# Kernel tuning notes

Hardware: AMD Instinct MI355X
Metric: run time of the kernel (lower is better)

The kernel has to match this reference:

```python
import jax, jax.numpy as jnp
import numpy as np


def setup_inputs() -> dict:
    key = jax.random.key(0)
    k1, k2, k3 = jax.random.split(key, 3)
    B, Cin, H, W = 64, 16, 256, 256
    Cout, K = 64, 3
    x = jax.random.normal(k1, (B, Cin, H, W), dtype=jnp.float32)
    # PyTorch Conv2d init scale ~ 1/sqrt(fan_in)
    fan_in = Cin * K * K
    conv_weight = jax.random.normal(k2, (Cout, Cin, K, K), dtype=jnp.float32) / np.sqrt(fan_in)
    conv_bias = jax.random.normal(k3, (Cout,), dtype=jnp.float32) / np.sqrt(fan_in)
    return {"x": x, "conv_weight": conv_weight, "conv_bias": conv_bias}


def reference(x, conv_weight, conv_bias):
    # Conv2d: stride=1, padding=0 (VALID), dilation=1, groups=1
    y = jax.lax.conv_general_dilated(
        x, conv_weight,
        window_strides=(1, 1),
        padding="VALID",
        dimension_numbers=("NCHW", "OIHW", "NCHW"),
    ) + conv_bias[None, :, None, None]          # [B, Cout, 254, 254]
    m = jnp.min(y, axis=1, keepdims=True)        # [B, 1, 254, 254] min over channels
    return jnp.tanh(jnp.tanh(m))                 # double tanh
```

## Files before the change

### kernel.cpp

```cpp
#include <hip/hip_runtime.h>
#include <math.h>

#define CIN    16
#define COUT   64
#define H      256
#define W      256
#define OH     254
#define OW     254
#define NTAP   9
#define NSTRIP 8
#define RING   6

typedef _Float16 f16x8  __attribute__((ext_vector_type(8)));
typedef float    f32x16 __attribute__((ext_vector_type(16)));

#define XSLOT(w, g) ((((w) << 1) | (g)) ^ (((w) >> 2) & 7))

__global__ void wpack_kernel(const float* __restrict__ w, _Float16* __restrict__ wpk) {
    int idx = blockIdx.x * 256 + threadIdx.x;
    if (idx >= NTAP * 2 * 64 * 8) return;
    int e = idx & 7, l = (idx >> 3) & 63, m = (idx >> 9) & 1, t = idx >> 10;
    int co  = (l & 31) + 32 * m;
    int cin = 8 * (l >> 5) + e;
    wpk[idx] = (_Float16)w[((co * CIN + cin) * 3 + t / 3) * 3 + (t % 3)];
}

__device__ __forceinline__ float tanh_fast(float v) {
    float e = __expf(2.0f * v);
    return 1.0f - 2.0f * __builtin_amdgcn_rcpf(e + 1.0f);
}

__global__ __launch_bounds__(256, 2) void conv_mfma_kernel(
        const float* __restrict__ x, const f16x8* __restrict__ wpk,
        const float* __restrict__ bias, float* __restrict__ out) {
    __shared__ f16x8 xs[RING * 512];
    __shared__ f16x8 wv[NTAP * 2 * 64];

    const int tid = threadIdx.x;
    int bid = blockIdx.x;
    int nb  = (bid & 7) * 64 + (bid >> 3);
    int b   = nb >> 3;
    int s   = nb & 7;
    const int npairs = (s == NSTRIP - 1) ? 15 : 16;
    const int oh0 = s * 32;

    const float* xb = x + (size_t)b * CIN * H * W;

    for (int i = tid; i < NTAP * 2 * 64; i += 256) wv[i] = wpk[i];

    const int rsel = tid >> 7;
    const int w2   = (tid & 127) * 2;

    #pragma unroll
    for (int pass = 0; pass < 2; ++pass) {
        int row = oh0 + 2 * pass + rsel;
        const float* p = xb + (size_t)row * W + w2;
        float2 vv[16];
        #pragma unroll
        for (int c = 0; c < 16; ++c) vv[c] = *(const float2*)(p + (size_t)c * H * W);
        int ring = 2 * pass + rsel;
        #pragma unroll
        for (int g = 0; g < 2; ++g)
            #pragma unroll
            for (int o = 0; o < 2; ++o) {
                f16x8 q;
                #pragma unroll
                for (int e = 0; e < 8; ++e)
                    q[e] = (_Float16)(o == 0 ? vv[8 * g + e].x : vv[8 * g + e].y);
                xs[ring * 512 + XSLOT(w2 + o, g)] = q;
            }
    }
    __syncthreads();

    const int lane = tid & 63;
    const int wave = tid >> 6;
    const int ohl  = wave >> 1;
    const int ph   = (wave & 1) * 128;
    const int l31  = lane & 31;
    const int g2   = lane >> 5;

    int off[3][4];
    #pragma unroll
    for (int kw = 0; kw < 3; ++kw)
        #pragma unroll
        for (int n = 0; n < 4; ++n) {
            int w = ph + 32 * n + l31 + kw;
            if (w > 255) w = 255;
            off[kw][n] = XSLOT(w, g2);
        }

    float binit[2][16];
    #pragma unroll
    for (int m = 0; m < 2; ++m)
        #pragma unroll
        for (int r = 0; r < 16; ++r)
            binit[m][r] = bias[(r & 3) + 8 * (r >> 2) + 4 * g2 + 32 * m];

    f32x16 acc[2][4];
    #pragma unroll
    for (int m = 0; m < 2; ++m)
        #pragma unroll
        for (int n = 0; n < 4; ++n)
            #pragma unroll
            for (int r = 0; r < 16; ++r)
                acc[m][n][r] = binit[m][r];

    for (int p = 0; p < npairs; ++p) {
        float2 vv[16];
        const bool pf = (p + 1 < npairs);
        if (pf) {
            int row = oh0 + 2 * p + 4 + rsel;
            const float* pp = xb + (size_t)row * W + w2;
            #pragma unroll
            for (int c = 0; c < 16; ++c) vv[c] = *(const float2*)(pp + (size_t)c * H * W);
        }

        int hb = 2 * p + ohl;
        int r0 = hb % RING, r1 = (hb + 1) % RING, r2 = (hb + 2) % RING;
        const f16x8* xr0 = xs + r0 * 512;
        const f16x8* xr1 = xs + r1 * 512;
        const f16x8* xr2 = xs + r2 * 512;

        #pragma unroll
        for (int t = 0; t < NTAP; ++t) {
            const int kh = t / 3, kw = t % 3;
            f16x8 a0 = wv[(t * 2 + 0) * 64 + lane];
            f16x8 a1 = wv[(t * 2 + 1) * 64 + lane];
            const f16x8* xr = (kh == 0) ? xr0 : (kh == 1) ? xr1 : xr2;
            #pragma unroll
            for (int n = 0; n < 4; ++n) {
                f16x8 bf = xr[off[kw][n]];
                acc[0][n] = __builtin_amdgcn_mfma_f32_32x32x16_f16(a0, bf, acc[0][n], 0, 0, 0);
                acc[1][n] = __builtin_amdgcn_mfma_f32_32x32x16_f16(a1, bf, acc[1][n], 0, 0, 0);
            }
        }

        const int oh = oh0 + 2 * p + ohl;
        #pragma unroll
        for (int n = 0; n < 4; ++n) {
            float mn = fminf(acc[0][n][0], acc[1][n][0]);
            #pragma unroll
            for (int r = 1; r < 16; ++r)
                mn = fminf(mn, fminf(acc[0][n][r], acc[1][n][r]));
            mn = fminf(mn, __shfl_xor(mn, 32));
            float t2 = tanh_fast(tanh_fast(mn));
            int px = ph + 32 * n + l31;
            if (g2 == 0 && px < OW)
                out[((size_t)b * OH + oh) * OW + px] = t2;
            #pragma unroll
            for (int m = 0; m < 2; ++m)
                #pragma unroll
                for (int r = 0; r < 16; ++r)
                    acc[m][n][r] = binit[m][r];
        }

        if (pf) {
            int ring = (2 * p + 4 + rsel) % RING;
            #pragma unroll
            for (int g = 0; g < 2; ++g)
                #pragma unroll
                for (int o = 0; o < 2; ++o) {
                    f16x8 q;
                    #pragma unroll
                    for (int e = 0; e < 8; ++e)
                        q[e] = (_Float16)(o == 0 ? vv[8 * g + e].x : vv[8 * g + e].y);
                    xs[ring * 512 + XSLOT(w2 + o, g)] = q;
                }
        }
        __syncthreads();
    }
}

extern "C" void kernel_launch(void* const* d_in, const int* in_sizes, int n_in,
                              void* d_out, int out_size, void* d_ws, size_t ws_size,
                              hipStream_t stream) {
    const float* x    = (const float*)d_in[0];
    const float* w    = (const float*)d_in[1];
    const float* bias = (const float*)d_in[2];
    float* out = (float*)d_out;
    _Float16* wpk = (_Float16*)d_ws;

    wpack_kernel<<<36, 256, 0, stream>>>(w, wpk);
    conv_mfma_kernel<<<512, 256, 0, stream>>>(x, (const f16x8*)wpk, bias, out);
}
```

Measured before the change: 100.8 us.

## Restructure conv into 512-thread blocks with deeper LDS ring and fewer barriers

Blocks grow to 512 threads, and each block now covers 64 output rows of one image, giving 256 blocks instead of 512. The LDS ring grows from 6 to 10 rows, so the block-wide barrier runs only every other row-pair iteration, and staging is split by channel group across half-blocks. Weight fragments are held in registers instead of being re-read from LDS on every tap. Each wave now computes two 32-pixel column tiles instead of four, which frees accumulator registers but halves MFMA work per B-fragment read and leaves fewer blocks to balance across CUs.

```diff
diff --git a/kernel.cpp b/kernel.cpp
--- a/kernel.cpp
+++ b/kernel.cpp
@@ -8,8 +8,7 @@
 #define OH     254
 #define OW     254
 #define NTAP   9
-#define NSTRIP 8
-#define RING   6
+#define RING   10
 
 typedef _Float16 f16x8  __attribute__((ext_vector_type(8)));
 typedef float    f32x16 __attribute__((ext_vector_type(16)));
@@ -30,116 +29,116 @@
     return 1.0f - 2.0f * __builtin_amdgcn_rcpf(e + 1.0f);
 }
 
-__global__ __launch_bounds__(256, 2) void conv_mfma_kernel(
+__global__ __launch_bounds__(512, 2) void conv_mfma_kernel(
         const float* __restrict__ x, const f16x8* __restrict__ wpk,
         const float* __restrict__ bias, float* __restrict__ out) {
-    __shared__ f16x8 xs[RING * 512];
-    __shared__ f16x8 wv[NTAP * 2 * 64];
+    __shared__ f16x8 xs[RING * 512 + 64];
 
     const int tid = threadIdx.x;
-    int bid = blockIdx.x;
-    int nb  = (bid & 7) * 64 + (bid >> 3);
-    int b   = nb >> 3;
-    int s   = nb & 7;
-    const int npairs = (s == NSTRIP - 1) ? 15 : 16;
-    const int oh0 = s * 32;
+    const int b   = blockIdx.x >> 2;
+    const int s   = blockIdx.x & 3;
+    const int oh0 = s * 64;
+    const int npairs = (s == 3) ? 31 : 32;
 
     const float* xb = x + (size_t)b * CIN * H * W;
 
-    for (int i = tid; i < NTAP * 2 * 64; i += 256) wv[i] = wpk[i];
+    const int lane = tid & 63;
+    f16x8 wreg[NTAP][2];
+#pragma unroll
+    for (int t = 0; t < NTAP; ++t)
+#pragma unroll
+        for (int m = 0; m < 2; ++m)
+            wreg[t][m] = wpk[(t * 2 + m) * 64 + lane];
 
-    const int rsel = tid >> 7;
-    const int w2   = (tid & 127) * 2;
+    const int gld  = tid >> 8;
+    const int rld  = (tid >> 7) & 1;
+    const int pp   = tid & 127;
+    const int w2   = pp * 2;
 
-    #pragma unroll
-    for (int pass = 0; pass < 2; ++pass) {
-        int row = oh0 + 2 * pass + rsel;
-        const float* p = xb + (size_t)row * W + w2;
-        float2 vv[16];
-        #pragma unroll
-        for (int c = 0; c < 16; ++c) vv[c] = *(const float2*)(p + (size_t)c * H * W);
-        int ring = 2 * pass + rsel;
-        #pragma unroll
-        for (int g = 0; g < 2; ++g)
-            #pragma unroll
-            for (int o = 0; o < 2; ++o) {
-                f16x8 q;
-                #pragma unroll
-                for (int e = 0; e < 8; ++e)
-                    q[e] = (_Float16)(o == 0 ? vv[8 * g + e].x : vv[8 * g + e].y);
-                xs[ring * 512 + XSLOT(w2 + o, g)] = q;
-            }
+#define STAGE(rowAbs, slot)                                                     \
+    {                                                                           \
+        int row_ = (rowAbs) > 255 ? 255 : (rowAbs);                             \
+        const float* p_ = xb + (size_t)row_ * W + w2;                           \
+        float2 vv_[8];                                                          \
+        _Pragma("unroll")                                                       \
+        for (int c = 0; c < 8; ++c)                                             \
+            vv_[c] = *(const float2*)(p_ + (size_t)(8 * gld + c) * (H * W));    \
+        f16x8 q0, q1;                                                           \
+        _Pragma("unroll")                                                       \
+        for (int c = 0; c < 8; ++c) { q0[c] = (_Float16)vv_[c].x;               \
+                                      q1[c] = (_Float16)vv_[c].y; }             \
+        xs[(slot) * 512 + XSLOT(w2,     gld)] = q0;                             \
+        xs[(slot) * 512 + XSLOT(w2 + 1, gld)] = q1;                             \
     }
+
+#pragma unroll
+    for (int i = 0; i < 3; ++i)
+        STAGE(oh0 + 2 * i + rld, 2 * i + rld)
     __syncthreads();
 
-    const int lane = tid & 63;
     const int wave = tid >> 6;
-    const int ohl  = wave >> 1;
-    const int ph   = (wave & 1) * 128;
+    const int ohl  = wave >> 2;
+    const int ph   = (wave & 3) * 64;
     const int l31  = lane & 31;
     const int g2   = lane >> 5;
 
-    int off[3][4];
-    #pragma unroll
+    int off[3][2];
+#pragma unroll
     for (int kw = 0; kw < 3; ++kw)
-        #pragma unroll
-        for (int n = 0; n < 4; ++n) {
+#pragma unroll
+        for (int n = 0; n < 2; ++n) {
             int w = ph + 32 * n + l31 + kw;
             if (w > 255) w = 255;
             off[kw][n] = XSLOT(w, g2);
         }
 
     float binit[2][16];
-    #pragma unroll
+#pragma unroll
     for (int m = 0; m < 2; ++m)
-        #pragma unroll
+#pragma unroll
         for (int r = 0; r < 16; ++r)
             binit[m][r] = bias[(r & 3) + 8 * (r >> 2) + 4 * g2 + 32 * m];
 
-    f32x16 acc[2][4];
-    #pragma unroll
+    f32x16 acc[2][2];
+#pragma unroll
     for (int m = 0; m < 2; ++m)
-        #pragma unroll
-        for (int n = 0; n < 4; ++n)
-            #pragma unroll
+#pragma unroll
+        for (int n = 0; n < 2; ++n)
+#pragma unroll
             for (int r = 0; r < 16; ++r)
                 acc[m][n][r] = binit[m][r];
 
     for (int p = 0; p < npairs; ++p) {
-        float2 vv[16];
-        const bool pf = (p + 1 < npairs);
-        if (pf) {
-            int row = oh0 + 2 * p + 4 + rsel;
-            const float* pp = xb + (size_t)row * W + w2;
-            #pragma unroll
-            for (int c = 0; c < 16; ++c) vv[c] = *(const float2*)(pp + (size_t)c * H * W);
-        }
+        int ldrow = oh0 + 2 * p + 6 + rld;
+        if (ldrow > 255) ldrow = 255;
+        const float* lp = xb + (size_t)ldrow * W + w2;
+        float2 vv[8];
+#pragma unroll
+        for (int c = 0; c < 8; ++c)
+            vv[c] = *(const float2*)(lp + (size_t)(8 * gld + c) * (H * W));
 
-        int hb = 2 * p + ohl;
-        int r0 = hb % RING, r1 = (hb + 1) % RING, r2 = (hb + 2) % RING;
-        const f16x8* xr0 = xs + r0 * 512;
-        const f16x8* xr1 = xs + r1 * 512;
-        const f16x8* xr2 = xs + r2 * 512;
+        const int hb = 2 * p + ohl;
+        const f16x8* xr0 = xs + (hb % RING) * 512;
+        const f16x8* xr1 = xs + ((hb + 1) % RING) * 512;
+        const f16x8* xr2 = xs + ((hb + 2) % RING) * 512;
 
-        #pragma unroll
+#pragma unroll
         for (int t = 0; t < NTAP; ++t) {
             const int kh = t / 3, kw = t % 3;
-            f16x8 a0 = wv[(t * 2 + 0) * 64 + lane];
-            f16x8 a1 = wv[(t * 2 + 1) * 64 + lane];
             const f16x8* xr = (kh == 0) ? xr0 : (kh == 1) ? xr1 : xr2;
-            #pragma unroll
-            for (int n = 0; n < 4; ++n) {
+#pragma unroll
+            for (int n = 0; n < 2; ++n) {
                 f16x8 bf = xr[off[kw][n]];
-                acc[0][n] = __builtin_amdgcn_mfma_f32_32x32x16_f16(a0, bf, acc[0][n], 0, 0, 0);
-                acc[1][n] = __builtin_amdgcn_mfma_f32_32x32x16_f16(a1, bf, acc[1][n], 0, 0, 0);
+                acc[0][n] = __builtin_amdgcn_mfma_f32_32x32x16_f16(wreg[t][0], bf, acc[0][n], 0, 0, 0);
+                acc[1][n] = __builtin_amdgcn_mfma_f32_32x32x16_f16(wreg[t][1], bf, acc[1][n], 0, 0, 0);
             }
         }
 
         const int oh = oh0 + 2 * p + ohl;
-        #pragma unroll
-        for (int n = 0; n < 4; ++n) {
+#pragma unroll
+        for (int n = 0; n < 2; ++n) {
             float mn = fminf(acc[0][n][0], acc[1][n][0]);
-            #pragma unroll
+#pragma unroll
             for (int r = 1; r < 16; ++r)
                 mn = fminf(mn, fminf(acc[0][n][r], acc[1][n][r]));
             mn = fminf(mn, __shfl_xor(mn, 32));
@@ -147,27 +146,24 @@
             int px = ph + 32 * n + l31;
             if (g2 == 0 && px < OW)
                 out[((size_t)b * OH + oh) * OW + px] = t2;
-            #pragma unroll
+#pragma unroll
             for (int m = 0; m < 2; ++m)
-                #pragma unroll
+#pragma unroll
                 for (int r = 0; r < 16; ++r)
                     acc[m][n][r] = binit[m][r];
         }
 
-        if (pf) {
-            int ring = (2 * p + 4 + rsel) % RING;
-            #pragma unroll
-            for (int g = 0; g < 2; ++g)
-                #pragma unroll
-                for (int o = 0; o < 2; ++o) {
-                    f16x8 q;
-                    #pragma unroll
-                    for (int e = 0; e < 8; ++e)
-                        q[e] = (_Float16)(o == 0 ? vv[8 * g + e].x : vv[8 * g + e].y);
-                    xs[ring * 512 + XSLOT(w2 + o, g)] = q;
-                }
+        {
+            const int slot = (2 * p + 6 + rld) % RING;
+            f16x8 q0, q1;
+#pragma unroll
+            for (int c = 0; c < 8; ++c) { q0[c] = (_Float16)vv[c].x;
+                                          q1[c] = (_Float16)vv[c].y; }
+            xs[slot * 512 + XSLOT(w2,     gld)] = q0;
+            xs[slot * 512 + XSLOT(w2 + 1, gld)] = q1;
         }
-        __syncthreads();
+
+        if (p & 1) __syncthreads();
     }
 }
 
@@ -181,5 +177,5 @@
     _Float16* wpk = (_Float16*)d_ws;
 
     wpack_kernel<<<36, 256, 0, stream>>>(w, wpk);
-    conv_mfma_kernel<<<512, 256, 0, stream>>>(x, (const f16x8*)wpk, bias, out);
+    conv_mfma_kernel<<<64 * 4, 512, 0, stream>>>(x, (const f16x8*)wpk, bias, out);
 }
```

Measured after the change: 93.43 us. -7.3%, faster.
